# Performance work log

Measured on AMD Instinct MI355X. Metric: run time of the kernel, lower is better.

Reference implementation:

```python
import jax, jax.numpy as jnp
import numpy as np
import math

DIM = 512


def setup_inputs() -> dict:
    key = jax.random.key(0)
    ks = jax.random.split(key, 6)
    B, N, D = 4, 4096, DIM
    H = D // 2
    features = jax.random.normal(ks[0], (B, N, D), dtype=jnp.float32)
    W1 = jax.random.normal(ks[1], (D, H), dtype=jnp.float32) * 0.02
    b1 = jnp.zeros((H,), dtype=jnp.float32)
    ln_g = jnp.ones((H,), dtype=jnp.float32)
    ln_b = jnp.zeros((H,), dtype=jnp.float32)
    W2 = jax.random.normal(ks[2], (H, 1), dtype=jnp.float32) * 0.02
    b2 = jnp.zeros((1,), dtype=jnp.float32)
    target_entropy = jnp.ones((1,), dtype=jnp.float32) * math.log(D)
    temperature = jnp.ones((1,), dtype=jnp.float32)
    return {"features": features, "W1": W1, "b1": b1, "ln_g": ln_g,
            "ln_b": ln_b, "W2": W2, "b2": b2,
            "target_entropy": target_entropy, "temperature": temperature}


def _layernorm(x, g, b, eps=1e-5):
    mu = jnp.mean(x, axis=-1, keepdims=True)
    var = jnp.mean((x - mu) ** 2, axis=-1, keepdims=True)
    return (x - mu) * jax.lax.rsqrt(var + eps) * g + b


def reference(features, W1, b1, ln_g, ln_b, W2, b2, target_entropy, temperature):
    # ---- compute_entropy: pairwise RBF kernel over [B, N, D] ----
    sq = jnp.sum(features ** 2, axis=-1)                       # [B, N]
    gram = jnp.einsum('bnd,bmd->bnm', features, features)      # [B, N, N]
    d2 = jnp.maximum(sq[:, :, None] + sq[:, None, :] - 2.0 * gram, 0.0)
    tau = temperature[0]
    kernel = jnp.exp(-d2 / (2.0 * tau ** 2))                   # [B, N, N]
    probs = kernel / jnp.sum(kernel, axis=-1, keepdims=True)
    entropy = -jnp.sum(probs * jnp.log(probs + 1e-6), axis=-1)  # [B, N]

    # ---- entropy estimator MLP (computed in original forward, output unused) ----
    h = features @ W1 + b1
    h = _layernorm(h, ln_g, ln_b)
    h = jax.nn.gelu(h, approximate=False)
    estimated_entropy = h @ W2 + b2                            # [B, N, 1] (unused)
    del estimated_entropy

    # ---- sigmoid-gated control signal ----
    entropy_diff = entropy - target_entropy[0]
    control_signal = jax.nn.sigmoid(-entropy_diff / tau)       # [B, N]
    controlled_features = features * control_signal[..., None]
    return controlled_features, control_signal
```

## Files before the change

### kernel.cpp

```cpp
#include <hip/hip_runtime.h>
#include <stdint.h>

#define N_TOK 4096
#define DIM   512
#define BATCH 4
#define BN    (BATCH * N_TOK)
#define JSPLIT 8
#define IPW   64
#define IPB   256
#define NG    (N_TOK / JSPLIT / 16)

typedef __attribute__((ext_vector_type(4))) float f32x4;
typedef __attribute__((ext_vector_type(8))) int   i32x8;

__device__ __forceinline__ float sumsq8(uint lo, uint hi) {
    float s = 0.f, f;
    f = __builtin_amdgcn_cvt_f32_fp8((int)lo, 0); s = fmaf(f, f, s);
    f = __builtin_amdgcn_cvt_f32_fp8((int)lo, 1); s = fmaf(f, f, s);
    f = __builtin_amdgcn_cvt_f32_fp8((int)lo, 2); s = fmaf(f, f, s);
    f = __builtin_amdgcn_cvt_f32_fp8((int)lo, 3); s = fmaf(f, f, s);
    f = __builtin_amdgcn_cvt_f32_fp8((int)hi, 0); s = fmaf(f, f, s);
    f = __builtin_amdgcn_cvt_f32_fp8((int)hi, 1); s = fmaf(f, f, s);
    f = __builtin_amdgcn_cvt_f32_fp8((int)hi, 2); s = fmaf(f, f, s);
    f = __builtin_amdgcn_cvt_f32_fp8((int)hi, 3); s = fmaf(f, f, s);
    return s;
}

__global__ __launch_bounds__(256) void prep_kernel(
    const float* __restrict__ feat, uint8_t* __restrict__ fb,
    uint8_t* __restrict__ fbT, float* __restrict__ sq)
{
    __shared__ __align__(16) long lt[1024];
    const int t = threadIdx.x;
    const int row16 = t >> 4, seg = t & 15;
    const size_t grp = blockIdx.x;
    const size_t row = grp * 16 + row16;

    const float4* src = (const float4*)(feat + row * DIM + seg * 32);
    uint32_t wd[8];
    float s = 0.f;
#pragma unroll
    for (int i = 0; i < 4; ++i) {
        float4 a = src[2 * i], b = src[2 * i + 1];
        uint lo = (uint)__builtin_amdgcn_cvt_pk_fp8_f32(a.x, a.y, 0, false);
        lo      = (uint)__builtin_amdgcn_cvt_pk_fp8_f32(a.z, a.w, (int)lo, true);
        uint hi = (uint)__builtin_amdgcn_cvt_pk_fp8_f32(b.x, b.y, 0, false);
        hi      = (uint)__builtin_amdgcn_cvt_pk_fp8_f32(b.z, b.w, (int)hi, true);
        wd[2 * i] = lo; wd[2 * i + 1] = hi;
        s += sumsq8(lo, hi);
    }

    uint4* dst = (uint4*)(fb + row * DIM + seg * 32);
    uint4 o0; o0.x = wd[0]; o0.y = wd[1]; o0.z = wd[2]; o0.w = wd[3];
    uint4 o1; o1.x = wd[4]; o1.y = wd[5]; o1.z = wd[6]; o1.w = wd[7];
    dst[0] = o0; dst[1] = o1;

#pragma unroll
    for (int i = 0; i < 4; ++i) {
        int c = seg * 4 + i;
        long d = ((long)(unsigned)wd[2 * i + 1] << 32) | (unsigned)wd[2 * i];
        lt[c * 16 + ((row16 + c) & 15)] = d;
    }

#pragma unroll
    for (int m = 1; m < 16; m <<= 1) s += __shfl_xor(s, m);
    if (seg == 0) sq[row] = s;

    __syncthreads();
    long* ot = (long*)(fbT + grp * 8192);
#pragma unroll
    for (int i = 0; i < 4; ++i) {
        int p   = t + i * 256;
        int kk  = p >> 8;
        int rem = p & 255;
        int q   = rem >> 6;
        int r   = (rem >> 2) & 15;
        int w8  = p & 3;
        int c   = kk * 16 + q * 4 + w8;
        ot[p] = lt[c * 16 + ((r + c) & 15)];
    }
}

__global__ __launch_bounds__(256, 2) void entropy_kernel(
    const uint8_t* __restrict__ fb, const uint8_t* __restrict__ fbT,
    const float* __restrict__ sq, const float* __restrict__ temp,
    float* __restrict__ Sp, float* __restrict__ Tp)
{
    const int t    = threadIdx.x;
    const int w    = t >> 6;
    const int lane = t & 63;
    const int q    = lane >> 4;
    const int c16  = lane & 15;

    const int flat  = blockIdx.x;
    const int combo = flat & 31;
    const int batch = combo >> 3;
    const int jh    = combo & 7;
    const int iblk  = flat >> 5;
    const int iw    = iblk * IPB + w * IPW;
    const size_t rowbase = (size_t)batch * N_TOK;

    const float tau    = temp[0];
    const float inv2t2 = 0.5f / (tau * tau);
    const float cg     = 1.0f / (tau * tau);

    i32x8 afrag[4][4];
#pragma unroll
    for (int s = 0; s < 4; ++s) {
        const uint4* ap = (const uint4*)(fb + (rowbase + iw + s * 16 + c16) * DIM);
#pragma unroll
        for (int kk = 0; kk < 4; ++kk) {
            uint4 lo = ap[kk * 8 + q * 2];
            uint4 hi = ap[kk * 8 + q * 2 + 1];
            i32x8 v = {(int)lo.x, (int)lo.y, (int)lo.z, (int)lo.w,
                       (int)hi.x, (int)hi.y, (int)hi.z, (int)hi.w};
            afrag[s][kk] = v;
        }
    }
    float pi[4][4];
#pragma unroll
    for (int s = 0; s < 4; ++s)
#pragma unroll
        for (int r = 0; r < 4; ++r)
            pi[s][r] = -sq[rowbase + iw + s * 16 + q * 4 + r] * inv2t2;

    float S[4][4], T[4][4];
#pragma unroll
    for (int s = 0; s < 4; ++s)
#pragma unroll
        for (int r = 0; r < 4; ++r) { S[s][r] = 0.f; T[s][r] = 0.f; }

    const uint4* bp = (const uint4*)(fbT
                    + ((size_t)batch * (N_TOK / 16) + (size_t)jh * NG) * 8192)
                    + q * 32 + c16 * 2;
    const float* sqj = sq + rowbase + jh * (N_TOK / JSPLIT) + c16;

    for (int g = 0; g < NG; ++g) {
        float pj = -sqj[g * 16] * inv2t2;
        const uint4* bg = bp + (size_t)g * 512;
        f32x4 acc[4] = {{0,0,0,0},{0,0,0,0},{0,0,0,0},{0,0,0,0}};
#pragma unroll
        for (int kk = 0; kk < 4; kk += 2) {
            uint4 l0 = bg[kk * 128],       h0 = bg[kk * 128 + 1];
            uint4 l1 = bg[(kk+1) * 128],   h1 = bg[(kk+1) * 128 + 1];
            i32x8 b0 = {(int)l0.x, (int)l0.y, (int)l0.z, (int)l0.w,
                        (int)h0.x, (int)h0.y, (int)h0.z, (int)h0.w};
            i32x8 b1 = {(int)l1.x, (int)l1.y, (int)l1.z, (int)l1.w,
                        (int)h1.x, (int)h1.y, (int)h1.z, (int)h1.w};
            acc[0] = __builtin_amdgcn_mfma_scale_f32_16x16x128_f8f6f4(afrag[0][kk], b0, acc[0], 0, 0, 0, 127, 0, 127);
            acc[1] = __builtin_amdgcn_mfma_scale_f32_16x16x128_f8f6f4(afrag[1][kk], b0, acc[1], 0, 0, 0, 127, 0, 127);
            acc[2] = __builtin_amdgcn_mfma_scale_f32_16x16x128_f8f6f4(afrag[2][kk], b0, acc[2], 0, 0, 0, 127, 0, 127);
            acc[3] = __builtin_amdgcn_mfma_scale_f32_16x16x128_f8f6f4(afrag[3][kk], b0, acc[3], 0, 0, 0, 127, 0, 127);
            acc[0] = __builtin_amdgcn_mfma_scale_f32_16x16x128_f8f6f4(afrag[0][kk+1], b1, acc[0], 0, 0, 0, 127, 0, 127);
            acc[1] = __builtin_amdgcn_mfma_scale_f32_16x16x128_f8f6f4(afrag[1][kk+1], b1, acc[1], 0, 0, 0, 127, 0, 127);
            acc[2] = __builtin_amdgcn_mfma_scale_f32_16x16x128_f8f6f4(afrag[2][kk+1], b1, acc[2], 0, 0, 0, 127, 0, 127);
            acc[3] = __builtin_amdgcn_mfma_scale_f32_16x16x128_f8f6f4(afrag[3][kk+1], b1, acc[3], 0, 0, 0, 127, 0, 127);
        }
        float m = -1e30f;
#pragma unroll
        for (int s = 0; s < 4; ++s)
#pragma unroll
            for (int r = 0; r < 4; ++r) {
                acc[s][r] = fmaf(acc[s][r], cg, pi[s][r] + pj);
                m = fmaxf(m, acc[s][r]);
            }
        if (m > -110.0f) {
#pragma unroll
            for (int s = 0; s < 4; ++s)
#pragma unroll
                for (int r = 0; r < 4; ++r) {
                    float ee = fminf(acc[s][r], 0.f);
                    float k  = __expf(ee);
                    S[s][r] += k;
                    T[s][r]  = fmaf(k, ee, T[s][r]);
                }
        }
    }

#pragma unroll
    for (int m = 1; m < 16; m <<= 1)
#pragma unroll
        for (int s = 0; s < 4; ++s)
#pragma unroll
            for (int r = 0; r < 4; ++r) {
                S[s][r] += __shfl_xor(S[s][r], m);
                T[s][r] += __shfl_xor(T[s][r], m);
            }

    if (c16 == 0) {
#pragma unroll
        for (int s = 0; s < 4; ++s)
#pragma unroll
            for (int r = 0; r < 4; ++r) {
                size_t idx = (size_t)jh * BN + rowbase + iw + s * 16 + q * 4 + r;
                Sp[idx] = S[s][r];
                Tp[idx] = T[s][r];
            }
    }
}

__global__ __launch_bounds__(256) void finalize_kernel(
    const float* __restrict__ feat, const float* __restrict__ Sp,
    const float* __restrict__ Tp, const float* __restrict__ tgt,
    const float* __restrict__ temp, float* __restrict__ out)
{
    int row  = (blockIdx.x << 2) + (threadIdx.x >> 6);
    int lane = threadIdx.x & 63;
    float S = 0.0f, T = 0.0f;
#pragma unroll
    for (int j = 0; j < JSPLIT; ++j) {
        S += Sp[(size_t)j * BN + row];
        T += Tp[(size_t)j * BN + row];
    }
    float tau = temp[0];
    float E  = __logf(S) - T / S;
    float cs = 1.0f / (1.0f + __expf((E - tgt[0]) / tau));

    const float4* F4 = (const float4*)(feat + (size_t)row * DIM);
    float4*       O4 = (float4*)(out + (size_t)row * DIM);
    float4 v0 = F4[lane], v1 = F4[lane + 64];
    v0.x *= cs; v0.y *= cs; v0.z *= cs; v0.w *= cs;
    v1.x *= cs; v1.y *= cs; v1.z *= cs; v1.w *= cs;
    O4[lane] = v0; O4[lane + 64] = v1;
    if (lane == 0) out[(size_t)BN * DIM + row] = cs;
}

extern "C" void kernel_launch(void* const* d_in, const int* in_sizes, int n_in,
                              void* d_out, int out_size, void* d_ws, size_t ws_size,
                              hipStream_t stream) {
    const float* feat = (const float*)d_in[0];
    const float* tgt  = (const float*)d_in[7];
    const float* temp = (const float*)d_in[8];
    float* out = (float*)d_out;

    char* ws = (char*)d_ws;
    uint8_t* fb  = (uint8_t*)ws;
    uint8_t* fbT = fb + (size_t)BN * DIM;
    float*   sq  = (float*)(fbT + (size_t)BN * DIM);
    float*   Sp  = sq + BN;
    float*   Tp  = Sp + (size_t)JSPLIT * BN;

    prep_kernel<<<dim3(BN / 16), dim3(256), 0, stream>>>(feat, fb, fbT, sq);
    entropy_kernel<<<dim3((N_TOK / IPB) * BATCH * JSPLIT), dim3(256), 0, stream>>>(fb, fbT, sq, temp, Sp, Tp);
    finalize_kernel<<<dim3(BN / 4), dim3(256), 0, stream>>>(feat, Sp, Tp, tgt, temp, out);
}
```

Before: 159.9 us.

## Fuse finalize into entropy kernel via last-block atomic counter

Removes the separate finalize kernel. The last of the JSPLIT blocks to finish a row block, detected with an atomic counter, sums the partials and writes the gated features and control signal. This saves one kernel launch and lets the output pass overlap with remaining entropy blocks. In exchange it adds a memset launch, and a single block per row group now does the 256-row scale loop serially, which could leave the tail underutilized.

```diff
diff --git a/kernel.cpp b/kernel.cpp
--- a/kernel.cpp
+++ b/kernel.cpp
@@ -82,10 +82,13 @@
 }
 
 __global__ __launch_bounds__(256, 2) void entropy_kernel(
-    const uint8_t* __restrict__ fb, const uint8_t* __restrict__ fbT,
-    const float* __restrict__ sq, const float* __restrict__ temp,
-    float* __restrict__ Sp, float* __restrict__ Tp)
+    const float* __restrict__ feat, const uint8_t* __restrict__ fb,
+    const uint8_t* __restrict__ fbT, const float* __restrict__ sq,
+    const float* __restrict__ tgt, const float* __restrict__ temp,
+    float* __restrict__ Sp, float* __restrict__ Tp,
+    int* __restrict__ cnt, float* __restrict__ out)
 {
+    __shared__ int sh_old;
     const int t    = threadIdx.x;
     const int w    = t >> 6;
     const int lane = t & 63;
@@ -193,36 +196,40 @@
 #pragma unroll
             for (int r = 0; r < 4; ++r) {
                 size_t idx = (size_t)jh * BN + rowbase + iw + s * 16 + q * 4 + r;
-                Sp[idx] = S[s][r];
-                Tp[idx] = T[s][r];
+                __hip_atomic_store(&Sp[idx], S[s][r], __ATOMIC_RELAXED, __HIP_MEMORY_SCOPE_AGENT);
+                __hip_atomic_store(&Tp[idx], T[s][r], __ATOMIC_RELAXED, __HIP_MEMORY_SCOPE_AGENT);
             }
     }
-}
-
-__global__ __launch_bounds__(256) void finalize_kernel(
-    const float* __restrict__ feat, const float* __restrict__ Sp,
-    const float* __restrict__ Tp, const float* __restrict__ tgt,
-    const float* __restrict__ temp, float* __restrict__ out)
-{
-    int row  = (blockIdx.x << 2) + (threadIdx.x >> 6);
-    int lane = threadIdx.x & 63;
-    float S = 0.0f, T = 0.0f;
-#pragma unroll
-    for (int j = 0; j < JSPLIT; ++j) {
-        S += Sp[(size_t)j * BN + row];
-        T += Tp[(size_t)j * BN + row];
-    }
-    float tau = temp[0];
-    float E  = __logf(S) - T / S;
-    float cs = 1.0f / (1.0f + __expf((E - tgt[0]) / tau));
-
-    const float4* F4 = (const float4*)(feat + (size_t)row * DIM);
-    float4*       O4 = (float4*)(out + (size_t)row * DIM);
-    float4 v0 = F4[lane], v1 = F4[lane + 64];
-    v0.x *= cs; v0.y *= cs; v0.z *= cs; v0.w *= cs;
-    v1.x *= cs; v1.y *= cs; v1.z *= cs; v1.w *= cs;
-    O4[lane] = v0; O4[lane + 64] = v1;
-    if (lane == 0) out[(size_t)BN * DIM + row] = cs;
+    __syncthreads();
+    if (t == 0) {
+        __threadfence();
+        sh_old = __hip_atomic_fetch_add(&cnt[batch * 16 + iblk], 1,
+                                        __ATOMIC_ACQ_REL, __HIP_MEMORY_SCOPE_AGENT);
+    }
+    __syncthreads();
+    if (sh_old != JSPLIT - 1) return;
+    __threadfence();
+
+    const float tgt0 = tgt[0];
+    for (int rr = 0; rr < 64; ++rr) {
+        size_t grow = rowbase + (size_t)iblk * IPB + w * 64 + rr;
+        float Ssum = 0.f, Tsum = 0.f;
+#pragma unroll
+        for (int j = 0; j < JSPLIT; ++j) {
+            Ssum += __hip_atomic_load(&Sp[(size_t)j * BN + grow], __ATOMIC_RELAXED, __HIP_MEMORY_SCOPE_AGENT);
+            Tsum += __hip_atomic_load(&Tp[(size_t)j * BN + grow], __ATOMIC_RELAXED, __HIP_MEMORY_SCOPE_AGENT);
+        }
+        float E  = __logf(Ssum) - Tsum / Ssum;
+        float cs = 1.0f / (1.0f + __expf((E - tgt0) / tau));
+
+        const float4* F4 = (const float4*)(feat + grow * DIM);
+        float4*       O4 = (float4*)(out + grow * DIM);
+        float4 v0 = F4[lane], v1 = F4[lane + 64];
+        v0.x *= cs; v0.y *= cs; v0.z *= cs; v0.w *= cs;
+        v1.x *= cs; v1.y *= cs; v1.z *= cs; v1.w *= cs;
+        O4[lane] = v0; O4[lane + 64] = v1;
+        if (lane == 0) out[(size_t)BN * DIM + grow] = cs;
+    }
 }
 
 extern "C" void kernel_launch(void* const* d_in, const int* in_sizes, int n_in,
@@ -239,8 +246,10 @@
     float*   sq  = (float*)(fbT + (size_t)BN * DIM);
     float*   Sp  = sq + BN;
     float*   Tp  = Sp + (size_t)JSPLIT * BN;
-
+    int*     cnt = (int*)(Tp + (size_t)JSPLIT * BN);
+
+    hipMemsetAsync(cnt, 0, BATCH * 16 * sizeof(int), stream);
     prep_kernel<<<dim3(BN / 16), dim3(256), 0, stream>>>(feat, fb, fbT, sq);
-    entropy_kernel<<<dim3((N_TOK / IPB) * BATCH * JSPLIT), dim3(256), 0, stream>>>(fb, fbT, sq, temp, Sp, Tp);
-    finalize_kernel<<<dim3(BN / 4), dim3(256), 0, stream>>>(feat, Sp, Tp, tgt, temp, out);
-}
+    entropy_kernel<<<dim3((N_TOK / IPB) * BATCH * JSPLIT), dim3(256), 0, stream>>>(
+        feat, fb, fbT, sq, tgt, temp, Sp, Tp, cnt, out);
+}
```

Measured after the change: 217.7 us. 36.2% more time.
